# Optimization experiments

Hardware: AMD Instinct MI355X
Metric: run time of the kernel (lower is better)

## Reference

```python
import jax, jax.numpy as jnp
import numpy as np

VOCAB = 25
HIDDEN = 512
OUT = 1000
BATCH = 64
SEQ = 512


def setup_inputs() -> dict:
    key = jax.random.key(0)
    ks = jax.random.split(key, 12)
    s_in = 1.0 / np.sqrt(HIDDEN)  # torch nn.RNN init scale U(-1/sqrt(H), 1/sqrt(H))
    def u(k, shape):
        return jax.random.uniform(k, shape, jnp.float32, -s_in, s_in)
    return {
        "x": jax.random.randint(ks[0], (BATCH, SEQ), 0, VOCAB, dtype=jnp.int64),
        "W_ih0": u(ks[1], (HIDDEN, VOCAB)),
        "W_hh0": u(ks[2], (HIDDEN, HIDDEN)),
        "b_ih0": u(ks[3], (HIDDEN,)),
        "b_hh0": u(ks[4], (HIDDEN,)),
        "W_ih1": u(ks[5], (HIDDEN, HIDDEN)),
        "W_hh1": u(ks[6], (HIDDEN, HIDDEN)),
        "b_ih1": u(ks[7], (HIDDEN,)),
        "b_hh1": u(ks[8], (HIDDEN,)),
        "W_out": u(ks[9], (OUT, HIDDEN)),
        "b_out": u(ks[10], (OUT,)),
    }


def _rnn_scan(xw, W_hh, b_hh):
    # xw: [B, T, H] = precomputed x @ W_ih^T + b_ih. Scan the tanh recurrence.
    B, T, H = xw.shape
    def step(h, xt):
        h = jnp.tanh(xt + h @ W_hh.T + b_hh)
        return h, h
    h0 = jnp.zeros((B, H), xw.dtype)
    _, hs = jax.lax.scan(step, h0, jnp.swapaxes(xw, 0, 1))  # [T, B, H]
    return jnp.swapaxes(hs, 0, 1)  # [B, T, H]


def reference(x, W_ih0, W_hh0, b_ih0, b_hh0, W_ih1, W_hh1, b_ih1, b_hh1, W_out, b_out):
    # one_hot(x) @ W_ih0^T == gather of columns of W_ih0 -> same math, no dense matmul
    xw0 = jnp.take(W_ih0.T, x, axis=0) + b_ih0          # [B, T, H]
    h1 = _rnn_scan(xw0, W_hh0, b_hh0)                    # layer 0 outputs
    xw1 = jnp.einsum('bth,oh->bto', h1, W_ih1) + b_ih1   # [B, T, H]
    h2 = _rnn_scan(xw1, W_hh1, b_hh1)                    # layer 1 outputs
    last = h2[:, -1, :]                                  # [B, H]
    return last @ W_out.T + b_out                        # [B, OUT]
```

## Files before the change

### kernel.cpp

```cpp
#include <hip/hip_runtime.h>


#define HD 512
#define BATCH 64
#define SEQ 512
#define NVOCAB 25
#define OUTD 1000
#define BH (BATCH * HD)
#define BHQ (BH / 4)
#define D1 8
#define LOGD1 3
#define D2 2
#define LOGD2 1
#define PSTRIDE 16
#define IS64_OFF 2048
#define HDR_INTS 4096
#define GUARD_MAX (1L << 23)

typedef unsigned short u16;
typedef unsigned int u32;
typedef unsigned long long u64;
typedef __attribute__((ext_vector_type(8))) _Float16 half8;
typedef __attribute__((ext_vector_type(4))) u32 u32x4;
typedef __attribute__((ext_vector_type(4))) float f32x4;

union Frag16 { u32x4 x; u64 q[2]; u16 h[8]; half8 v; };

__device__ __forceinline__ u16 f2h(float f) {
    union { _Float16 h; u16 u; } c; c.h = (_Float16)f; return c.u;
}
__device__ __forceinline__ u64 ld64a(const u64* p) {
    return __hip_atomic_load((u64*)p, __ATOMIC_RELAXED, __HIP_MEMORY_SCOPE_AGENT);
}
__device__ __forceinline__ void st64a(u64* p, u64 v) {
    __hip_atomic_store(p, v, __ATOMIC_RELAXED, __HIP_MEMORY_SCOPE_AGENT);
}
__device__ __forceinline__ int ld32a(const int* p) {
    return __hip_atomic_load((int*)p, __ATOMIC_RELAXED, __HIP_MEMORY_SCOPE_AGENT);
}
#define LDX4(dst, addr) \
    asm volatile("global_load_dwordx4 %0, %1, off sc0" : "=v"(dst) : "v"(addr))
#define WAITV0() do { \
    asm volatile("s_waitcnt vmcnt(0)" ::: "memory"); \
    __builtin_amdgcn_sched_barrier(0); \
} while (0)

__device__ __forceinline__ u64 pack_tag(const u16 hv[4], u32 tag) {
    return ((u64)(((u32)hv[0] & 0xFFFEu) | tag))
         | ((u64)hv[1] << 16) | ((u64)hv[2] << 32) | ((u64)hv[3] << 48);
}

__global__ void init_kernel(int* hdr, u64* h1, u64* h2, const int* x32) {
    long i = (long)blockIdx.x * 256 + threadIdx.x;
    if (i < HDR_INTS) {
        if (i == IS64_OFF) {
            int all0 = 1;
            for (int j = 0; j < 64; ++j) if (x32[2 * j + 1] != 0) all0 = 0;
            hdr[i] = all0;
        } else hdr[i] = 0;
    } else {
        long r = i - HDR_INTS;
        if (r < (long)D1 * BHQ) h1[r] = (r < BHQ) ? 0ull : 1ull;
        else {
            long s = r - (long)D1 * BHQ;
            if (s < (long)D2 * BHQ) h2[s] = (s < BHQ) ? 0ull : 1ull;
        }
    }
}

__global__ __launch_bounds__(128, 1) void rnn_fused(
    const float* __restrict__ Whh0, const float* __restrict__ Wih0,
    const int* __restrict__ x,
    const float* __restrict__ bih0, const float* __restrict__ bhh0,
    const float* __restrict__ Whh1, const float* __restrict__ Wih1,
    const float* __restrict__ bih1, const float* __restrict__ bhh1,
    u64* h1ring, u64* h2ring, float* h2final, int* hdr)
{
    int* prog = hdr;
    const int tid  = threadIdx.x;
    const int wv   = tid >> 6;
    const int lane = tid & 63;
    const int quad = lane >> 4;
    const int l16  = lane & 15;
    const int layer = blockIdx.x >> 6;
    const int w     = blockIdx.x & 63;
    const int rbig  = w >> 2;
    const int cg    = w & 3;
    const int u     = rbig * 2 + wv;
    const int rowbase = u * 16;
    const int arow = rowbase + l16;
    const int row0 = rowbase + quad * 4;
    const int col  = cg * 16 + l16;
    const int pg = lane & 31;
    const size_t repoff = (size_t)(cg * 16 + (pg & 15)) * 128 + pg * 4 + (pg & 3);

    const float* Wself = layer ? Whh1 : Whh0;
    half8 Ah[16];
    #pragma unroll
    for (int kc = 0; kc < 16; ++kc) {
        Frag16 th;
        #pragma unroll
        for (int j = 0; j < 8; ++j)
            th.h[j] = f2h(Wself[arow * HD + kc * 32 + quad * 8 + j]);
        Ah[kc] = th.v;
    }
    half8 Aw[16];
    if (layer) {
        #pragma unroll
        for (int kc = 0; kc < 16; ++kc) {
            Frag16 th;
            #pragma unroll
            for (int j = 0; j < 8; ++j)
                th.h[j] = f2h(Wih1[arow * HD + kc * 32 + quad * 8 + j]);
            Aw[kc] = th.v;
        }
    }
    const float* bA = layer ? bih1 : bih0;
    const float* bB = layer ? bhh1 : bhh0;
    float bsum[4];
    #pragma unroll
    for (int i = 0; i < 4; ++i) bsum[i] = bA[row0 + i] + bB[row0 + i];
    const int is64 = hdr[IS64_OFF];

    long guard = 0;
    int pv = 0;

    for (int t = 0; t < SEQ; ++t) {
        if (layer == 0) {
            int xi = is64 ? (int)((const long long*)x)[col * SEQ + t]
                          : x[col * SEQ + t];
            float wx[4];
            #pragma unroll
            for (int i = 0; i < 4; ++i) wx[i] = Wih0[(row0 + i) * NVOCAB + xi];
            const int need = t + 1 - D1;
            if (need > 0) {
                bool stale = (lane < 32) && (pv < need);
                if (__ballot(stale) != 0ULL && stale)
                    pv = ld32a(prog + (cg * 32 + lane) * PSTRIDE);
            }
            const int sl = t & (D1 - 1);
            const u32 ex = (u32)((t >> LOGD1) & 1);
            const u64* sb = h1ring + (size_t)sl * BHQ;
            {
                const u64* rep = sb + repoff;
                for (;;) {
                    u32 bad = (((u32)ld64a(rep)) ^ ex) & 1u;
                    if (__ballot(bad != 0) == 0ULL) break;
                    if (++guard > GUARD_MAX) break;
                    __builtin_amdgcn_s_sleep(1);
                }
            }
            const u64* pb = sb + (size_t)col * 128 + quad * 2;
            Frag16 B[16];
            for (;;) {
                #pragma unroll
                for (int kc = 0; kc < 16; ++kc) LDX4(B[kc].x, pb + kc * 8);
                WAITV0();
                u32 bad = 0;
                #pragma unroll
                for (int kc = 0; kc < 16; ++kc)
                    bad |= ((((u32)B[kc].q[0]) ^ ex) | (((u32)B[kc].q[1]) ^ ex)) & 1u;
                if (__ballot(bad != 0) == 0ULL) break;
                if (++guard > GUARD_MAX) break;
            }
            f32x4 a0 = {0.f, 0.f, 0.f, 0.f}, a1 = a0;
            #pragma unroll
            for (int kc = 0; kc < 16; kc += 2) {
                a0 = __builtin_amdgcn_mfma_f32_16x16x32_f16(Ah[kc],     B[kc].v,     a0, 0, 0, 0);
                a1 = __builtin_amdgcn_mfma_f32_16x16x32_f16(Ah[kc + 1], B[kc + 1].v, a1, 0, 0, 0);
            }
            float hf[4]; u16 hv[4];
            #pragma unroll
            for (int i = 0; i < 4; ++i) {
                float pre = a0[i] + a1[i] + bsum[i] + wx[i];
                hf[i] = tanhf(pre); hv[i] = f2h(hf[i]);
            }
            if (need > 0) {
                while (__ballot((lane < 32) && (pv < need)) != 0ULL) {
                    if ((lane < 32) && (pv < need))
                        pv = ld32a(prog + (cg * 32 + lane) * PSTRIDE);
                    if (++guard > GUARD_MAX) break;
                }
            }
            const int wsl = (t + 1) & (D1 - 1);
            const u32 wtg = (u32)(((t + 1) >> LOGD1) & 1);
            st64a(h1ring + (size_t)wsl * BHQ + col * 128 + (row0 >> 2),
                  pack_tag(hv, wtg));
        } else {
            const int s2 = t & (D2 - 1);
            const u32 e2 = (u32)((t >> LOGD2) & 1);
            const int s1 = (t + 1) & (D1 - 1);
            const u32 e1 = (u32)(((t + 1) >> LOGD1) & 1);
            const u64* b2 = h2ring + (size_t)s2 * BHQ;
            const u64* b1 = h1ring + (size_t)s1 * BHQ;
            {
                const u64* rep = (lane < 32) ? (b2 + repoff) : (b1 + repoff);
                const u32 exr = (lane < 32) ? e2 : e1;
                for (;;) {
                    u32 bad = (((u32)ld64a(rep)) ^ exr) & 1u;
                    if (__ballot(bad != 0) == 0ULL) break;
                    if (++guard > GUARD_MAX) break;
                    __builtin_amdgcn_s_sleep(1);
                }
            }
            const u64* pb2 = b2 + (size_t)col * 128 + quad * 2;
            const u64* pb1 = b1 + (size_t)col * 128 + quad * 2;
            Frag16 B2[16], B1[16];
            for (;;) {
                #pragma unroll
                for (int kc = 0; kc < 16; ++kc) {
                    LDX4(B2[kc].x, pb2 + kc * 8);
                    LDX4(B1[kc].x, pb1 + kc * 8);
                }
                WAITV0();
                u32 bad = 0;
                #pragma unroll
                for (int kc = 0; kc < 16; ++kc) {
                    bad |= ((((u32)B2[kc].q[0]) ^ e2) | (((u32)B2[kc].q[1]) ^ e2)) & 1u;
                    bad |= ((((u32)B1[kc].q[0]) ^ e1) | (((u32)B1[kc].q[1]) ^ e1)) & 1u;
                }
                if (__ballot(bad != 0) == 0ULL) break;
                if (++guard > GUARD_MAX) break;
            }
            if (lane == 0) {
                int pubv = t + 1;
                u32 dep = (u32)B1[0].q[0];
                asm volatile("" : "+v"(pubv) : "v"(dep));
                __hip_atomic_store(prog + (cg * 32 + u) * PSTRIDE, pubv,
                                   __ATOMIC_RELAXED, __HIP_MEMORY_SCOPE_AGENT);
            }
            f32x4 aS0 = {0.f, 0.f, 0.f, 0.f}, aS1 = aS0, aI0 = aS0, aI1 = aS0;
            #pragma unroll
            for (int kc = 0; kc < 16; kc += 2) {
                aS0 = __builtin_amdgcn_mfma_f32_16x16x32_f16(Ah[kc],     B2[kc].v,     aS0, 0, 0, 0);
                aS1 = __builtin_amdgcn_mfma_f32_16x16x32_f16(Ah[kc + 1], B2[kc + 1].v, aS1, 0, 0, 0);
                aI0 = __builtin_amdgcn_mfma_f32_16x16x32_f16(Aw[kc],     B1[kc].v,     aI0, 0, 0, 0);
                aI1 = __builtin_amdgcn_mfma_f32_16x16x32_f16(Aw[kc + 1], B1[kc + 1].v, aI1, 0, 0, 0);
            }
            float hf[4]; u16 hv[4];
            #pragma unroll
            for (int i = 0; i < 4; ++i) {
                float pre = aS0[i] + aS1[i] + aI0[i] + aI1[i] + bsum[i];
                hf[i] = tanhf(pre); hv[i] = f2h(hf[i]);
            }
            const int wsl = (t + 1) & (D2 - 1);
            const u32 wtg = (u32)(((t + 1) >> LOGD2) & 1);
            st64a(h2ring + (size_t)wsl * BHQ + col * 128 + (row0 >> 2),
                  pack_tag(hv, wtg));
            if (t == SEQ - 1)
                *(f32x4*)(h2final + col * HD + row0) = *(f32x4*)hf;
        }
    }
}

__global__ __launch_bounds__(256) void out_kernel(
    const float* __restrict__ h2last, const float* __restrict__ Wout,
    const float* __restrict__ bout, float* __restrict__ out)
{
    int o = blockIdx.x * 256 + threadIdx.x;
    int b = blockIdx.y;
    if (o >= OUTD) return;
    const float* hrow = h2last + b * HD;
    const float* wrow = Wout + o * HD;
    float acc = 0.f;
    for (int k = 0; k < HD; k += 4) {
        float4 hv = *(const float4*)(hrow + k);
        float4 wv = *(const float4*)(wrow + k);
        acc += hv.x * wv.x + hv.y * wv.y + hv.z * wv.z + hv.w * wv.w;
    }
    out[b * OUTD + o] = acc + bout[o];
}

extern "C" void kernel_launch(void* const* d_in, const int* in_sizes, int n_in,
                              void* d_out, int out_size, void* d_ws, size_t ws_size,
                              hipStream_t stream) {
    const int*   x     = (const int*)d_in[0];
    const float* W_ih0 = (const float*)d_in[1];
    const float* W_hh0 = (const float*)d_in[2];
    const float* b_ih0 = (const float*)d_in[3];
    const float* b_hh0 = (const float*)d_in[4];
    const float* W_ih1 = (const float*)d_in[5];
    const float* W_hh1 = (const float*)d_in[6];
    const float* b_ih1 = (const float*)d_in[7];
    const float* b_hh1 = (const float*)d_in[8];
    const float* W_out = (const float*)d_in[9];
    const float* b_out = (const float*)d_in[10];

    const size_t needed = (size_t)HDR_INTS * 4 + (size_t)D1 * BHQ * 8
                        + (size_t)D2 * BHQ * 8 + (size_t)BH * 4;
    if (ws_size < needed) return;

    int* hdr = (int*)d_ws;
    u64* h1ring = (u64*)((char*)d_ws + (size_t)HDR_INTS * 4);
    u64* h2ring = h1ring + (size_t)D1 * BHQ;
    float* h2final = (float*)(h2ring + (size_t)D2 * BHQ);

    const long ninit = HDR_INTS + (long)(D1 + D2) * BHQ;
    init_kernel<<<(int)((ninit + 255) / 256), 256, 0, stream>>>(hdr, h1ring, h2ring, x);
    rnn_fused<<<128, 128, 0, stream>>>(W_hh0, W_ih0, x, b_ih0, b_hh0,
                                       W_hh1, W_ih1, b_ih1, b_hh1,
                                       h1ring, h2ring, h2final, hdr);
    out_kernel<<<dim3(4, BATCH), 256, 0, stream>>>(h2final, W_out, b_out, (float*)d_out);
}
```

Before: 2.080 ms.

## Fuse both RNN layers into one lockstep wavefront with double-buffered rings

Each of 128 single-wave blocks now computes both layer-0 step t and layer-1 step t-1, running one extra iteration to finish layer 1. The depth-8 ring with explicit progress counters is replaced by two-slot rings for both layers, so a single combined wait covers both dependencies. This drops the cross-layer progress bookkeeping and the skewed producer/consumer pipeline. In exchange, each step's critical path now holds both layers' MFMA work serially, and every wave keeps three weight matrices in registers, which raises register pressure.

```diff
diff --git a/kernel.cpp b/kernel.cpp
--- a/kernel.cpp
+++ b/kernel.cpp
@@ -8,11 +8,6 @@
 #define OUTD 1000
 #define BH (BATCH * HD)
 #define BHQ (BH / 4)
-#define D1 8
-#define LOGD1 3
-#define D2 2
-#define LOGD2 1
-#define PSTRIDE 16
 #define IS64_OFF 2048
 #define HDR_INTS 4096
 #define GUARD_MAX (1L << 23)
@@ -34,9 +29,6 @@
 }
 __device__ __forceinline__ void st64a(u64* p, u64 v) {
     __hip_atomic_store(p, v, __ATOMIC_RELAXED, __HIP_MEMORY_SCOPE_AGENT);
-}
-__device__ __forceinline__ int ld32a(const int* p) {
-    return __hip_atomic_load((int*)p, __ATOMIC_RELAXED, __HIP_MEMORY_SCOPE_AGENT);
 }
 #define LDX4(dst, addr) \
     asm volatile("global_load_dwordx4 %0, %1, off sc0" : "=v"(dst) : "v"(addr))
@@ -60,15 +52,12 @@
         } else hdr[i] = 0;
     } else {
         long r = i - HDR_INTS;
-        if (r < (long)D1 * BHQ) h1[r] = (r < BHQ) ? 0ull : 1ull;
-        else {
-            long s = r - (long)D1 * BHQ;
-            if (s < (long)D2 * BHQ) h2[s] = (s < BHQ) ? 0ull : 1ull;
-        }
-    }
-}
-
-__global__ __launch_bounds__(128, 1) void rnn_fused(
+        if (r < 2L * BHQ) h1[r] = (r < BHQ) ? 0ull : 1ull;
+        else if (r < 4L * BHQ) h2[r - 2L * BHQ] = 1ull;
+    }
+}
+
+__global__ __launch_bounds__(64, 1) void rnn_fused(
     const float* __restrict__ Whh0, const float* __restrict__ Wih0,
     const int* __restrict__ x,
     const float* __restrict__ bih0, const float* __restrict__ bhh0,
@@ -76,17 +65,11 @@
     const float* __restrict__ bih1, const float* __restrict__ bhh1,
     u64* h1ring, u64* h2ring, float* h2final, int* hdr)
 {
-    int* prog = hdr;
-    const int tid  = threadIdx.x;
-    const int wv   = tid >> 6;
-    const int lane = tid & 63;
+    const int lane = threadIdx.x & 63;
     const int quad = lane >> 4;
     const int l16  = lane & 15;
-    const int layer = blockIdx.x >> 6;
-    const int w     = blockIdx.x & 63;
-    const int rbig  = w >> 2;
-    const int cg    = w & 3;
-    const int u     = rbig * 2 + wv;
+    const int u    = (int)blockIdx.x >> 2;
+    const int cg   = (int)blockIdx.x & 3;
     const int rowbase = u * 16;
     const int arow = rowbase + l16;
     const int row0 = rowbase + quad * 4;
@@ -94,160 +77,107 @@
     const int pg = lane & 31;
     const size_t repoff = (size_t)(cg * 16 + (pg & 15)) * 128 + pg * 4 + (pg & 3);
 
-    const float* Wself = layer ? Whh1 : Whh0;
-    half8 Ah[16];
+    half8 A0[16], A1[16], Aw[16];
     #pragma unroll
     for (int kc = 0; kc < 16; ++kc) {
-        Frag16 th;
+        Frag16 t0, t1, tw;
         #pragma unroll
-        for (int j = 0; j < 8; ++j)
-            th.h[j] = f2h(Wself[arow * HD + kc * 32 + quad * 8 + j]);
-        Ah[kc] = th.v;
-    }
-    half8 Aw[16];
-    if (layer) {
+        for (int j = 0; j < 8; ++j) {
+            const int widx = arow * HD + kc * 32 + quad * 8 + j;
+            t0.h[j] = f2h(Whh0[widx]);
+            t1.h[j] = f2h(Whh1[widx]);
+            tw.h[j] = f2h(Wih1[widx]);
+        }
+        A0[kc] = t0.v; A1[kc] = t1.v; Aw[kc] = tw.v;
+    }
+    float bs0[4], bs1[4];
+    #pragma unroll
+    for (int i = 0; i < 4; ++i) {
+        bs0[i] = bih0[row0 + i] + bhh0[row0 + i];
+        bs1[i] = bih1[row0 + i] + bhh1[row0 + i];
+    }
+    const int is64 = hdr[IS64_OFF];
+
+    long guard = 0;
+
+    for (int t = 0; t <= SEQ; ++t) {
+        const int tt = (t < SEQ) ? t : (SEQ - 1);
+        int xi = is64 ? (int)((const long long*)x)[col * SEQ + tt]
+                      : x[col * SEQ + tt];
+        float wx[4];
         #pragma unroll
-        for (int kc = 0; kc < 16; ++kc) {
-            Frag16 th;
-            #pragma unroll
-            for (int j = 0; j < 8; ++j)
-                th.h[j] = f2h(Wih1[arow * HD + kc * 32 + quad * 8 + j]);
-            Aw[kc] = th.v;
-        }
-    }
-    const float* bA = layer ? bih1 : bih0;
-    const float* bB = layer ? bhh1 : bhh0;
-    float bsum[4];
-    #pragma unroll
-    for (int i = 0; i < 4; ++i) bsum[i] = bA[row0 + i] + bB[row0 + i];
-    const int is64 = hdr[IS64_OFF];
-
-    long guard = 0;
-    int pv = 0;
-
-    for (int t = 0; t < SEQ; ++t) {
-        if (layer == 0) {
-            int xi = is64 ? (int)((const long long*)x)[col * SEQ + t]
-                          : x[col * SEQ + t];
-            float wx[4];
-            #pragma unroll
-            for (int i = 0; i < 4; ++i) wx[i] = Wih0[(row0 + i) * NVOCAB + xi];
-            const int need = t + 1 - D1;
-            if (need > 0) {
-                bool stale = (lane < 32) && (pv < need);
-                if (__ballot(stale) != 0ULL && stale)
-                    pv = ld32a(prog + (cg * 32 + lane) * PSTRIDE);
-            }
-            const int sl = t & (D1 - 1);
-            const u32 ex = (u32)((t >> LOGD1) & 1);
-            const u64* sb = h1ring + (size_t)sl * BHQ;
-            {
-                const u64* rep = sb + repoff;
-                for (;;) {
-                    u32 bad = (((u32)ld64a(rep)) ^ ex) & 1u;
-                    if (__ballot(bad != 0) == 0ULL) break;
-                    if (++guard > GUARD_MAX) break;
-                    __builtin_amdgcn_s_sleep(1);
-                }
-            }
-            const u64* pb = sb + (size_t)col * 128 + quad * 2;
-            Frag16 B[16];
+        for (int i = 0; i < 4; ++i) wx[i] = Wih0[(row0 + i) * NVOCAB + xi];
+
+        const int rs = t & 1;
+        const u32 e1 = (u32)((t >> 1) & 1);
+        const u32 e2 = (u32)(((t + 2) >> 1) & 1);
+        const u64* sb1 = h1ring + (size_t)rs * BHQ;
+        const u64* sb2 = h2ring + (size_t)rs * BHQ;
+        {
+            const u64* rep = (lane < 32) ? (sb1 + repoff) : (sb2 + repoff);
+            const u32 exr = (lane < 32) ? e1 : e2;
             for (;;) {
-                #pragma unroll
-                for (int kc = 0; kc < 16; ++kc) LDX4(B[kc].x, pb + kc * 8);
-                WAITV0();
-                u32 bad = 0;
-                #pragma unroll
-                for (int kc = 0; kc < 16; ++kc)
-                    bad |= ((((u32)B[kc].q[0]) ^ ex) | (((u32)B[kc].q[1]) ^ ex)) & 1u;
+                u32 bad = (((u32)ld64a(rep)) ^ exr) & 1u;
                 if (__ballot(bad != 0) == 0ULL) break;
                 if (++guard > GUARD_MAX) break;
-            }
-            f32x4 a0 = {0.f, 0.f, 0.f, 0.f}, a1 = a0;
+                __builtin_amdgcn_s_sleep(1);
+            }
+        }
+        const u64* pb1 = sb1 + (size_t)col * 128 + quad * 2;
+        const u64* pb2 = sb2 + (size_t)col * 128 + quad * 2;
+        Frag16 B1[16], B2[16];
+        for (;;) {
+            #pragma unroll
+            for (int kc = 0; kc < 16; ++kc) {
+                LDX4(B1[kc].x, pb1 + kc * 8);
+                LDX4(B2[kc].x, pb2 + kc * 8);
+            }
+            WAITV0();
+            u32 bad = 0;
+            #pragma unroll
+            for (int kc = 0; kc < 16; ++kc) {
+                bad |= ((((u32)B1[kc].q[0]) ^ e1) | (((u32)B1[kc].q[1]) ^ e1)) & 1u;
+                bad |= ((((u32)B2[kc].q[0]) ^ e2) | (((u32)B2[kc].q[1]) ^ e2)) & 1u;
+            }
+            if (__ballot(bad != 0) == 0ULL) break;
+            if (++guard > GUARD_MAX) break;
+        }
+        const int ws = (t + 1) & 1;
+        if (t < SEQ) {
+            f32x4 aH0 = {0.f, 0.f, 0.f, 0.f}, aH1 = aH0;
             #pragma unroll
             for (int kc = 0; kc < 16; kc += 2) {
-                a0 = __builtin_amdgcn_mfma_f32_16x16x32_f16(Ah[kc],     B[kc].v,     a0, 0, 0, 0);
-                a1 = __builtin_amdgcn_mfma_f32_16x16x32_f16(Ah[kc + 1], B[kc + 1].v, a1, 0, 0, 0);
+                aH0 = __builtin_amdgcn_mfma_f32_16x16x32_f16(A0[kc],     B1[kc].v,     aH0, 0, 0, 0);
+                aH1 = __builtin_amdgcn_mfma_f32_16x16x32_f16(A0[kc + 1], B1[kc + 1].v, aH1, 0, 0, 0);
             }
             float hf[4]; u16 hv[4];
             #pragma unroll
             for (int i = 0; i < 4; ++i) {
-                float pre = a0[i] + a1[i] + bsum[i] + wx[i];
+                float pre = aH0[i] + aH1[i] + bs0[i] + wx[i];
                 hf[i] = tanhf(pre); hv[i] = f2h(hf[i]);
             }
-            if (need > 0) {
-                while (__ballot((lane < 32) && (pv < need)) != 0ULL) {
-                    if ((lane < 32) && (pv < need))
-                        pv = ld32a(prog + (cg * 32 + lane) * PSTRIDE);
-                    if (++guard > GUARD_MAX) break;
-                }
-            }
-            const int wsl = (t + 1) & (D1 - 1);
-            const u32 wtg = (u32)(((t + 1) >> LOGD1) & 1);
-            st64a(h1ring + (size_t)wsl * BHQ + col * 128 + (row0 >> 2),
-                  pack_tag(hv, wtg));
-        } else {
-            const int s2 = t & (D2 - 1);
-            const u32 e2 = (u32)((t >> LOGD2) & 1);
-            const int s1 = (t + 1) & (D1 - 1);
-            const u32 e1 = (u32)(((t + 1) >> LOGD1) & 1);
-            const u64* b2 = h2ring + (size_t)s2 * BHQ;
-            const u64* b1 = h1ring + (size_t)s1 * BHQ;
-            {
-                const u64* rep = (lane < 32) ? (b2 + repoff) : (b1 + repoff);
-                const u32 exr = (lane < 32) ? e2 : e1;
-                for (;;) {
-                    u32 bad = (((u32)ld64a(rep)) ^ exr) & 1u;
-                    if (__ballot(bad != 0) == 0ULL) break;
-                    if (++guard > GUARD_MAX) break;
-                    __builtin_amdgcn_s_sleep(1);
-                }
-            }
-            const u64* pb2 = b2 + (size_t)col * 128 + quad * 2;
-            const u64* pb1 = b1 + (size_t)col * 128 + quad * 2;
-            Frag16 B2[16], B1[16];
-            for (;;) {
-                #pragma unroll
-                for (int kc = 0; kc < 16; ++kc) {
-                    LDX4(B2[kc].x, pb2 + kc * 8);
-                    LDX4(B1[kc].x, pb1 + kc * 8);
-                }
-                WAITV0();
-                u32 bad = 0;
-                #pragma unroll
-                for (int kc = 0; kc < 16; ++kc) {
-                    bad |= ((((u32)B2[kc].q[0]) ^ e2) | (((u32)B2[kc].q[1]) ^ e2)) & 1u;
-                    bad |= ((((u32)B1[kc].q[0]) ^ e1) | (((u32)B1[kc].q[1]) ^ e1)) & 1u;
-                }
-                if (__ballot(bad != 0) == 0ULL) break;
-                if (++guard > GUARD_MAX) break;
-            }
-            if (lane == 0) {
-                int pubv = t + 1;
-                u32 dep = (u32)B1[0].q[0];
-                asm volatile("" : "+v"(pubv) : "v"(dep));
-                __hip_atomic_store(prog + (cg * 32 + u) * PSTRIDE, pubv,
-                                   __ATOMIC_RELAXED, __HIP_MEMORY_SCOPE_AGENT);
-            }
+            st64a(h1ring + (size_t)ws * BHQ + (size_t)col * 128 + (row0 >> 2),
+                  pack_tag(hv, (u32)(((t + 1) >> 1) & 1)));
+        }
+        if (t >= 1) {
             f32x4 aS0 = {0.f, 0.f, 0.f, 0.f}, aS1 = aS0, aI0 = aS0, aI1 = aS0;
             #pragma unroll
             for (int kc = 0; kc < 16; kc += 2) {
-                aS0 = __builtin_amdgcn_mfma_f32_16x16x32_f16(Ah[kc],     B2[kc].v,     aS0, 0, 0, 0);
-                aS1 = __builtin_amdgcn_mfma_f32_16x16x32_f16(Ah[kc + 1], B2[kc + 1].v, aS1, 0, 0, 0);
+                aS0 = __builtin_amdgcn_mfma_f32_16x16x32_f16(A1[kc],     B2[kc].v,     aS0, 0, 0, 0);
+                aS1 = __builtin_amdgcn_mfma_f32_16x16x32_f16(A1[kc + 1], B2[kc + 1].v, aS1, 0, 0, 0);
                 aI0 = __builtin_amdgcn_mfma_f32_16x16x32_f16(Aw[kc],     B1[kc].v,     aI0, 0, 0, 0);
                 aI1 = __builtin_amdgcn_mfma_f32_16x16x32_f16(Aw[kc + 1], B1[kc + 1].v, aI1, 0, 0, 0);
             }
             float hf[4]; u16 hv[4];
             #pragma unroll
             for (int i = 0; i < 4; ++i) {
-                float pre = aS0[i] + aS1[i] + aI0[i] + aI1[i] + bsum[i];
+                float pre = aS0[i] + aS1[i] + aI0[i] + aI1[i] + bs1[i];
                 hf[i] = tanhf(pre); hv[i] = f2h(hf[i]);
             }
-            const int wsl = (t + 1) & (D2 - 1);
-            const u32 wtg = (u32)(((t + 1) >> LOGD2) & 1);
-            st64a(h2ring + (size_t)wsl * BHQ + col * 128 + (row0 >> 2),
-                  pack_tag(hv, wtg));
-            if (t == SEQ - 1)
+            if (t < SEQ)
+                st64a(h2ring + (size_t)ws * BHQ + (size_t)col * 128 + (row0 >> 2),
+                      pack_tag(hv, (u32)(((t + 3) >> 1) & 1)));
+            else
                 *(f32x4*)(h2final + col * HD + row0) = *(f32x4*)hf;
         }
     }
@@ -286,19 +216,18 @@
     const float* W_out = (const float*)d_in[9];
     const float* b_out = (const float*)d_in[10];
 
-    const size_t needed = (size_t)HDR_INTS * 4 + (size_t)D1 * BHQ * 8
-                        + (size_t)D2 * BHQ * 8 + (size_t)BH * 4;
+    const size_t needed = (size_t)HDR_INTS * 4 + 4ULL * BHQ * 8 + (size_t)BH * 4;
     if (ws_size < needed) return;
 
     int* hdr = (int*)d_ws;
     u64* h1ring = (u64*)((char*)d_ws + (size_t)HDR_INTS * 4);
-    u64* h2ring = h1ring + (size_t)D1 * BHQ;
-    float* h2final = (float*)(h2ring + (size_t)D2 * BHQ);
-
-    const long ninit = HDR_INTS + (long)(D1 + D2) * BHQ;
+    u64* h2ring = h1ring + 2ULL * BHQ;
+    float* h2final = (float*)(h2ring + 2ULL * BHQ);
+
+    const long ninit = HDR_INTS + 4L * BHQ;
     init_kernel<<<(int)((ninit + 255) / 256), 256, 0, stream>>>(hdr, h1ring, h2ring, x);
-    rnn_fused<<<128, 128, 0, stream>>>(W_hh0, W_ih0, x, b_ih0, b_hh0,
-                                       W_hh1, W_ih1, b_ih1, b_hh1,
-                                       h1ring, h2ring, h2final, hdr);
+    rnn_fused<<<128, 64, 0, stream>>>(W_hh0, W_ih0, x, b_ih0, b_hh0,
+                                      W_hh1, W_ih1, b_ih1, b_hh1,
+                                      h1ring, h2ring, h2final, hdr);
     out_kernel<<<dim3(4, BATCH), 256, 0, stream>>>(h2final, W_out, b_out, (float*)d_out);
 }
```

Result: faster. 1.841 ms (-11.5%).
